# Kernel optimization log

Measured on AMD Instinct MI355X. Metric: run time of the kernel, lower is better.

Reference implementation:

```python
import jax, jax.numpy as jnp
import numpy as np

N, E, G, L = 50000, 800000, 256, 3
D, NF, EF, OUT = 300, 128, 16, 128
BN_EPS = 1e-5


def setup_inputs() -> dict:
    key = jax.random.key(0)
    ks = jax.random.split(key, 24)
    s = 0.02
    inp = {
        "node_feat": jax.random.normal(ks[0], (N, NF), jnp.float32),
        "edge_feat": jax.random.normal(ks[1], (E, EF), jnp.float32),
        "src": jax.random.randint(ks[2], (E,), 0, N),
        "dst": jax.random.randint(ks[3], (E,), 0, N),
        "graph_ids": jnp.sort(jax.random.randint(ks[4], (N,), 0, G)),
        "num_graphs": G,
        # encoder params
        "node_W": jax.random.normal(ks[5], (NF, D), jnp.float32) * s,
        "node_b": jnp.zeros((D,), jnp.float32),
        # per-layer edge encoders [L, EF, D]
        "edge_W": jax.random.normal(ks[6], (L, EF, D), jnp.float32) * s,
        "edge_b": jnp.zeros((L, D), jnp.float32),
        # per-layer GINEConv MLP: Linear(D,2D) BN ReLU Linear(2D,D) BN
        "W1": jax.random.normal(ks[7], (L, D, 2 * D), jnp.float32) * s,
        "b1": jnp.zeros((L, 2 * D), jnp.float32),
        "g1": jnp.ones((L, 2 * D), jnp.float32),
        "beta1": jnp.zeros((L, 2 * D), jnp.float32),
        "W2": jax.random.normal(ks[8], (L, 2 * D, D), jnp.float32) * s,
        "b2": jnp.zeros((L, D), jnp.float32),
        "g2": jnp.ones((L, D), jnp.float32),
        "beta2": jnp.zeros((L, D), jnp.float32),
        # prediction head
        "pred_W": jax.random.normal(ks[9], (D, OUT), jnp.float32) * s,
        "pred_b": jnp.zeros((OUT,), jnp.float32),
    }
    return inp


def _bn(x, g, b):
    # BatchNorm1d in training mode: biased batch statistics
    m = jnp.mean(x, axis=0)
    v = jnp.var(x, axis=0)
    return (x - m) * jax.lax.rsqrt(v + BN_EPS) * g + b


def reference(node_feat, edge_feat, src, dst, graph_ids, num_graphs,
              node_W, node_b, edge_W, edge_b,
              W1, b1, g1, beta1, W2, b2, g2, beta2,
              pred_W, pred_b):
    n_nodes = node_feat.shape[0]
    n_layers = edge_W.shape[0]
    hn = node_feat @ node_W + node_b  # [N, D]
    for l in range(n_layers):
        he = edge_feat @ edge_W[l] + edge_b[l]            # [E, D]
        msg = jax.nn.relu(hn[src] + he)                   # gather + edge fuse
        agg = jax.ops.segment_sum(msg, dst, num_segments=n_nodes)
        h = hn + agg                                      # (1+eps)*h + agg, eps=0
        h = jax.nn.relu(_bn(h @ W1[l] + b1[l], g1[l], beta1[l]))
        h = _bn(h @ W2[l] + b2[l], g2[l], beta2[l])
        hn = jax.nn.relu(h) if l != n_layers - 1 else h   # dropout p=0 -> identity
    # AvgPooling over nodes per graph
    cnt = jax.ops.segment_sum(jnp.ones((n_nodes, 1), hn.dtype), graph_ids,
                              num_segments=num_graphs)
    hg = jax.ops.segment_sum(hn, graph_ids, num_segments=num_graphs)
    hg = hg / jnp.maximum(cnt, 1.0)
    return hg @ pred_W + pred_b  # [G, OUT]
```

## Files before the change

### kernel.cpp

```cpp
#include <hip/hip_runtime.h>
#include <hip/hip_fp16.h>

#define N_NODES 50000
#define N_EDGES 800000
#define N_GRAPHS 256
#define N_LAYERS 3
#define DIM 300
#define NFEAT 128
#define EFEAT 16
#define OUTD 128
#define BN_EPS 1e-5f
#define HSTRIDE 320

typedef __attribute__((ext_vector_type(8))) _Float16 hfrag8;
typedef __attribute__((ext_vector_type(4))) float facc4;
typedef __attribute__((ext_vector_type(4))) unsigned short us4;
typedef __attribute__((ext_vector_type(8))) unsigned short us8;
typedef __attribute__((ext_vector_type(4))) unsigned int ui4;

__device__ __forceinline__ unsigned short f2bf(float f) {
    unsigned u = __float_as_uint(f);
    unsigned r = ((u >> 16) & 1u) + 0x7fffu;
    return (unsigned short)((u + r) >> 16);
}
__device__ __forceinline__ float bf2f(unsigned short h) {
    return __uint_as_float(((unsigned)h) << 16);
}
__device__ __forceinline__ unsigned short f2h(float f) {
    return __half_as_ushort(__float2half(f));
}
__device__ __forceinline__ float h2f(unsigned short u) {
    return __half2float(__ushort_as_half(u));
}

#if __has_builtin(__builtin_amdgcn_fdot2_f32_bf16)
#define GATHER_DOT2 1
typedef __attribute__((ext_vector_type(2))) __bf16 bf16x2_t;
__device__ __forceinline__ float dot2bf(unsigned a, unsigned b, float c) {
    return __builtin_amdgcn_fdot2_f32_bf16(
        __builtin_bit_cast(bf16x2_t, a), __builtin_bit_cast(bf16x2_t, b), c, false);
}
#else
#define GATHER_DOT2 0
#endif

__device__ __forceinline__ void load_lds16(const void* gsrc, void* ldsdst) {
    __builtin_amdgcn_global_load_lds(
        (const __attribute__((address_space(1))) unsigned int*)gsrc,
        (__attribute__((address_space(3))) unsigned int*)ldsdst,
        16, 0, 0);
}

#define MFMAH(a, b, c) __builtin_amdgcn_mfma_f32_16x16x32_f16(a, b, c, 0, 0, 0)

__global__ __launch_bounds__(256) void toh4(
    const float* __restrict__ x, unsigned short* __restrict__ H, int n4)
{
    int i = blockIdx.x * 256 + threadIdx.x;
    if (i >= n4) return;
    float4 v = ((const float4*)x)[i];
    us4 h;
    h.x = f2h(v.x); h.y = f2h(v.y); h.z = f2h(v.z); h.w = f2h(v.w);
    ((us4*)H)[i] = h;
}

__global__ __launch_bounds__(256) void toh_row(
    const float* __restrict__ hn, unsigned short* __restrict__ hnb)
{
    int i = blockIdx.x * 256 + threadIdx.x;
    if (i >= N_NODES * 80) return;
    int row = i / 80;
    int q = i - row * 80;
    us4 o;
    if (q < 75) {
        float4 v = *(const float4*)&hn[(size_t)row * DIM + 4 * q];
        o.x = f2h(v.x); o.y = f2h(v.y); o.z = f2h(v.z); o.w = f2h(v.w);
    } else {
        o.x = 0; o.y = 0; o.z = 0; o.w = 0;
    }
    *(us4*)&hnb[(size_t)row * HSTRIDE + 4 * q] = o;
}

__global__ __launch_bounds__(256) void conv_wt(
    const float* __restrict__ W, unsigned short* __restrict__ H,
    int K, int N, int Kp, int Np)
{
    int idx = blockIdx.x * 256 + threadIdx.x;
    if (idx >= Np * Kp) return;
    int n = idx / Kp;
    int k = idx - n * Kp;
    float v = (n < N && k < K) ? W[(size_t)k * N + n] : 0.f;
    H[idx] = f2h(v);
}

__global__ __launch_bounds__(256, 2) void gemm_pp(
    const unsigned short* __restrict__ Ah, const unsigned short* __restrict__ Bt,
    const float* __restrict__ bias, float* __restrict__ C,
    int M, int N, int Kp, float* __restrict__ stats)
{
    __shared__ unsigned short lds[8192];
    const int tid = threadIdx.x;
    const int lane = tid & 63;
    const int w = tid >> 6;
    const int m0 = blockIdx.y * 128;
    const int n0 = blockIdx.x * 128;
    const int wm = (w & 1) * 64;
    const int wn = (w >> 1) * 64;

    const int srow = lane >> 2;
    const int scol = (lane & 3) * 8;

    const unsigned short* gp[4];
    unsigned loff[4];
#pragma unroll
    for (int i = 0; i < 4; ++i) {
        int c = w * 4 + i;
        const unsigned short* pl = (c < 8) ? Ah : Bt;
        int rowg;
        if (c < 8) {
            rowg = m0 + (c & 7) * 16 + srow;
            rowg = min(rowg, M - 1);
        } else {
            rowg = n0 + (c & 7) * 16 + srow;
        }
        gp[i] = pl + (size_t)rowg * Kp + scol;
        loff[i] = c * 512;
    }

    facc4 acc[4][4];
    facc4 zero = {0.f, 0.f, 0.f, 0.f};
#pragma unroll
    for (int i = 0; i < 4; ++i)
#pragma unroll
        for (int j = 0; j < 4; ++j) acc[i][j] = zero;

    const int fr = lane & 15;
    const int fq = (lane >> 4) * 8;

    for (int k0 = 0; k0 < Kp; k0 += 32) {
#pragma unroll
        for (int i = 0; i < 4; ++i) {
            load_lds16(gp[i], &lds[loff[i]]);
            gp[i] += 32;
        }
        __syncthreads();

        hfrag8 ah[4], bh[4];
#pragma unroll
        for (int t = 0; t < 4; ++t) {
            int ar = wm + t * 16 + fr;
            ah[t] = *(const hfrag8*)&lds[ar * 32 + fq];
            int br = wn + t * 16 + fr;
            bh[t] = *(const hfrag8*)&lds[4096 + br * 32 + fq];
        }
#pragma unroll
        for (int i = 0; i < 4; ++i)
#pragma unroll
            for (int j = 0; j < 4; ++j)
                acc[i][j] = MFMAH(ah[i], bh[j], acc[i][j]);
        __syncthreads();
    }

#pragma unroll
    for (int i = 0; i < 4; ++i)
#pragma unroll
        for (int j = 0; j < 4; ++j) {
            int col = n0 + wn + j * 16 + (lane & 15);
            if (col >= N) continue;
            float bv = bias[col];
#pragma unroll
            for (int r = 0; r < 4; ++r) {
                int row = m0 + wm + i * 16 + (lane >> 4) * 4 + r;
                if (row < M)
                    C[(size_t)row * N + col] = acc[i][j][r] + bv;
            }
        }

    if (stats != nullptr) {
#pragma unroll
        for (int j = 0; j < 4; ++j) {
            int col = n0 + wn + j * 16 + (lane & 15);
            float cs = 0.f, cq = 0.f;
            if (col < N) {
                float bv = bias[col];
#pragma unroll
                for (int i = 0; i < 4; ++i)
#pragma unroll
                    for (int r = 0; r < 4; ++r) {
                        int row = m0 + wm + i * 16 + (lane >> 4) * 4 + r;
                        if (row < M) {
                            float y = acc[i][j][r] + bv;
                            cs += y;
                            cq = fmaf(y, y, cq);
                        }
                    }
            }
            cs += __shfl_xor(cs, 16, 64); cq += __shfl_xor(cq, 16, 64);
            cs += __shfl_xor(cs, 32, 64); cq += __shfl_xor(cq, 32, 64);
            if ((lane >> 4) == 0 && col < N) {
                atomicAdd(&stats[col], cs);
                atomicAdd(&stats[N + col], cq);
            }
        }
    }
}

__global__ __launch_bounds__(256, 2) void gemm_af(
    const float* __restrict__ A, const unsigned short* __restrict__ Bt,
    const float* __restrict__ bias, float* __restrict__ C,
    int M, int N, int K, int Kp,
    const float* __restrict__ abn, float* __restrict__ stats)
{
    __shared__ unsigned short lds[8192];
    const int tid = threadIdx.x;
    const int lane = tid & 63;
    const int w = tid >> 6;
    const int m0 = blockIdx.y * 128;
    const int n0 = blockIdx.x * 128;
    const int wm = (w & 1) * 64;
    const int wn = (w >> 1) * 64;

    const int srow = lane >> 2;
    const int scol = (lane & 3) * 8;

    const unsigned short* gpb[2];
    unsigned loffb[2];
#pragma unroll
    for (int i = 0; i < 2; ++i) {
        int c = w * 2 + i;
        int rowg = n0 + c * 16 + srow;
        gpb[i] = Bt + (size_t)rowg * Kp + scol;
        loffb[i] = 4096 + c * 512;
    }

    facc4 acc[4][4];
    facc4 zero = {0.f, 0.f, 0.f, 0.f};
#pragma unroll
    for (int i = 0; i < 4; ++i)
#pragma unroll
        for (int j = 0; j < 4; ++j) acc[i][j] = zero;

    const int fr = lane & 15;
    const int fq = (lane >> 4) * 8;

    for (int k0 = 0; k0 < Kp; k0 += 32) {
#pragma unroll
        for (int i = 0; i < 2; ++i) {
            load_lds16(gpb[i], &lds[loffb[i]]);
            gpb[i] += 32;
        }
#pragma unroll
        for (int i = 0; i < 4; ++i) {
            int idx = tid + i * 256;
            int row = idx >> 3;
            int q4 = idx & 7;
            int rg = min(m0 + row, M - 1);
            int kk = k0 + q4 * 4;
            us4 h;
            if (kk < K) {
                float4 v = *(const float4*)&A[(size_t)rg * K + kk];
                float4 sa = *(const float4*)&abn[kk];
                float4 sb = *(const float4*)&abn[K + kk];
                h.x = f2h(fmaxf(fmaf(v.x, sa.x, sb.x), 0.f));
                h.y = f2h(fmaxf(fmaf(v.y, sa.y, sb.y), 0.f));
                h.z = f2h(fmaxf(fmaf(v.z, sa.z, sb.z), 0.f));
                h.w = f2h(fmaxf(fmaf(v.w, sa.w, sb.w), 0.f));
            } else {
                h.x = 0; h.y = 0; h.z = 0; h.w = 0;
            }
            *(us4*)&lds[row * 32 + q4 * 4] = h;
        }
        __syncthreads();

        hfrag8 ah[4], bh[4];
#pragma unroll
        for (int t = 0; t < 4; ++t) {
            int ar = wm + t * 16 + fr;
            ah[t] = *(const hfrag8*)&lds[ar * 32 + fq];
            int br = wn + t * 16 + fr;
            bh[t] = *(const hfrag8*)&lds[4096 + br * 32 + fq];
        }
#pragma unroll
        for (int i = 0; i < 4; ++i)
#pragma unroll
            for (int j = 0; j < 4; ++j)
                acc[i][j] = MFMAH(ah[i], bh[j], acc[i][j]);
        __syncthreads();
    }

#pragma unroll
    for (int i = 0; i < 4; ++i)
#pragma unroll
        for (int j = 0; j < 4; ++j) {
            int col = n0 + wn + j * 16 + (lane & 15);
            if (col >= N) continue;
            float bv = bias[col];
#pragma unroll
            for (int r = 0; r < 4; ++r) {
                int row = m0 + wm + i * 16 + (lane >> 4) * 4 + r;
                if (row < M)
                    C[(size_t)row * N + col] = acc[i][j][r] + bv;
            }
        }

    if (stats != nullptr) {
#pragma unroll
        for (int j = 0; j < 4; ++j) {
            int col = n0 + wn + j * 16 + (lane & 15);
            float cs = 0.f, cq = 0.f;
            if (col < N) {
                float bv = bias[col];
#pragma unroll
                for (int i = 0; i < 4; ++i)
#pragma unroll
                    for (int r = 0; r < 4; ++r) {
                        int row = m0 + wm + i * 16 + (lane >> 4) * 4 + r;
                        if (row < M) {
                            float y = acc[i][j][r] + bv;
                            cs += y;
                            cq = fmaf(y, y, cq);
                        }
                    }
            }
            cs += __shfl_xor(cs, 16, 64); cq += __shfl_xor(cq, 16, 64);
            cs += __shfl_xor(cs, 32, 64); cq += __shfl_xor(cq, 32, 64);
            if ((lane >> 4) == 0 && col < N) {
                atomicAdd(&stats[col], cs);
                atomicAdd(&stats[N + col], cq);
            }
        }
    }
}

__global__ __launch_bounds__(256) void csr_count(const int* __restrict__ dst, int* __restrict__ P)
{
    int e = blockIdx.x * 256 + threadIdx.x;
    if (e < N_EDGES) atomicAdd(&P[dst[e] + 1], 1);
}

__global__ __launch_bounds__(1024) void csr_scan(int* __restrict__ P)
{
    __shared__ int part[1024];
    const int t = threadIdx.x;
    const int CH = 49;
    int i0 = t * CH;
    int s = 0;
    for (int i = i0; i < i0 + CH; ++i) {
        if (i <= N_NODES) { s += P[i]; P[i] = s; }
    }
    part[t] = s;
    __syncthreads();
    if (t == 0) {
        int run = 0;
        for (int k = 0; k < 1024; ++k) { int tmp = part[k]; part[k] = run; run += tmp; }
    }
    __syncthreads();
    int off = part[t];
    for (int i = i0; i < i0 + CH; ++i) {
        if (i <= N_NODES) P[i] += off;
    }
}

__global__ __launch_bounds__(256) void csr_fill(
    const int* __restrict__ dst, int* __restrict__ P, int* __restrict__ eids)
{
    int e = blockIdx.x * 256 + threadIdx.x;
    if (e < N_EDGES) {
        int pos = atomicAdd(&P[dst[e]], 1);
        eids[pos] = e;
    }
}

__global__ __launch_bounds__(256) void edge_pack_bf(
    const int* __restrict__ src, const int* __restrict__ eids,
    const float* __restrict__ edge_feat, int* __restrict__ es,
    unsigned short* __restrict__ efsb)
{
    int j = blockIdx.x * 256 + threadIdx.x;
    if (j >= N_EDGES) return;
    int e = eids[j];
    es[j] = src[e];
    const float* sp = edge_feat + (size_t)e * EFEAT;
    us8 o0, o1;
#pragma unroll
    for (int k = 0; k < 8; ++k) {
        o0[k] = f2bf(sp[k]);
        o1[k] = f2bf(sp[8 + k]);
    }
    *(us8*)&efsb[(size_t)j * EFEAT] = o0;
    *(us8*)&efsb[(size_t)j * EFEAT + 8] = o1;
}

__global__ __launch_bounds__(256) void gather_agg7(
    const unsigned short* __restrict__ hnb, const unsigned short* __restrict__ efsb,
    const int* __restrict__ es, const int* __restrict__ P,
    const float* __restrict__ eW, const float* __restrict__ eb,
    unsigned short* __restrict__ aggH)
{
    const int v = blockIdx.x * 4 + (threadIdx.x >> 6);
    if (v >= N_NODES) return;
    const int lane = threadIdx.x & 63;

    float acc[5];
    float ebv[5];
    {
        us4 r4 = *(const us4*)&hnb[(size_t)v * HSTRIDE + 4 * lane];
        acc[0] = h2f(r4.x); acc[1] = h2f(r4.y);
        acc[2] = h2f(r4.z); acc[3] = h2f(r4.w);
        acc[4] = h2f(hnb[(size_t)v * HSTRIDE + 256 + lane]);
    }
#if GATHER_DOT2
    unsigned wpk[8][5];
#pragma unroll
    for (int q = 0; q < 5; ++q) {
        int d = (q < 4) ? 4 * lane + q : 256 + lane;
        bool dv = d < DIM;
        ebv[q] = dv ? eb[d] : 0.f;
#pragma unroll
        for (int p = 0; p < 8; ++p) {
            unsigned short h0 = dv ? f2bf(eW[(2 * p) * DIM + d]) : (unsigned short)0;
            unsigned short h1 = dv ? f2bf(eW[(2 * p + 1) * DIM + d]) : (unsigned short)0;
            wpk[p][q] = (unsigned)h0 | ((unsigned)h1 << 16);
        }
    }
#else
    float wr[EFEAT][5];
#pragma unroll
    for (int q = 0; q < 5; ++q) {
        int d = (q < 4) ? 4 * lane + q : 256 + lane;
        bool dv = d < DIM;
        ebv[q] = dv ? eb[d] : 0.f;
#pragma unroll
        for (int k = 0; k < EFEAT; ++k)
            wr[k][q] = dv ? eW[k * DIM + d] : 0.f;
    }
#endif

    const int j0 = (v == 0) ? 0 : P[v - 1];
    const int j1 = P[v];

    int j = j0;
    for (; j + 4 <= j1; j += 4) {
        int s0 = __builtin_amdgcn_readfirstlane(es[j]);
        int s1 = __builtin_amdgcn_readfirstlane(es[j + 1]);
        int s2 = __builtin_amdgcn_readfirstlane(es[j + 2]);
        int s3 = __builtin_amdgcn_readfirstlane(es[j + 3]);
        const unsigned short* __restrict__ h0 = hnb + (size_t)s0 * HSTRIDE;
        const unsigned short* __restrict__ h1 = hnb + (size_t)s1 * HSTRIDE;
        const unsigned short* __restrict__ h2p = hnb + (size_t)s2 * HSTRIDE;
        const unsigned short* __restrict__ h3 = hnb + (size_t)s3 * HSTRIDE;
        us4 r4[4];
        unsigned short r1[4];
        r4[0] = *(const us4*)&h0[4 * lane];  r1[0] = h0[256 + lane];
        r4[1] = *(const us4*)&h1[4 * lane];  r1[1] = h1[256 + lane];
        r4[2] = *(const us4*)&h2p[4 * lane]; r1[2] = h2p[256 + lane];
        r4[3] = *(const us4*)&h3[4 * lane];  r1[3] = h3[256 + lane];
#if GATHER_DOT2
        ui4 pa[4][2];
#pragma unroll
        for (int u = 0; u < 4; ++u) {
            pa[u][0] = *(const ui4*)&efsb[(size_t)(j + u) * EFEAT];
            pa[u][1] = *(const ui4*)&efsb[(size_t)(j + u) * EFEAT + 8];
        }
#pragma unroll
        for (int u = 0; u < 4; ++u) {
            float hv[5];
            hv[0] = h2f(r4[u][0]); hv[1] = h2f(r4[u][1]);
            hv[2] = h2f(r4[u][2]); hv[3] = h2f(r4[u][3]);
            hv[4] = h2f(r1[u]);
#pragma unroll
            for (int q = 0; q < 5; ++q) {
                float he = ebv[q];
                he = dot2bf(pa[u][0][0], wpk[0][q], he);
                he = dot2bf(pa[u][0][1], wpk[1][q], he);
                he = dot2bf(pa[u][0][2], wpk[2][q], he);
                he = dot2bf(pa[u][0][3], wpk[3][q], he);
                he = dot2bf(pa[u][1][0], wpk[4][q], he);
                he = dot2bf(pa[u][1][1], wpk[5][q], he);
                he = dot2bf(pa[u][1][2], wpk[6][q], he);
                he = dot2bf(pa[u][1][3], wpk[7][q], he);
                acc[q] += fmaxf(hv[q] + he, 0.f);
            }
        }
#else
        us8 pk[4][2];
#pragma unroll
        for (int u = 0; u < 4; ++u) {
            pk[u][0] = *(const us8*)&efsb[(size_t)(j + u) * EFEAT];
            pk[u][1] = *(const us8*)&efsb[(size_t)(j + u) * EFEAT + 8];
        }
#pragma unroll
        for (int u = 0; u < 4; ++u) {
            float hv[5];
            hv[0] = h2f(r4[u][0]); hv[1] = h2f(r4[u][1]);
            hv[2] = h2f(r4[u][2]); hv[3] = h2f(r4[u][3]);
            hv[4] = h2f(r1[u]);
            float ef[EFEAT];
#pragma unroll
            for (int k = 0; k < 8; ++k) {
                ef[k] = bf2f(pk[u][0][k]);
                ef[8 + k] = bf2f(pk[u][1][k]);
            }
#pragma unroll
            for (int q = 0; q < 5; ++q) {
                float he = ebv[q];
#pragma unroll
                for (int k = 0; k < EFEAT; ++k) he = fmaf(ef[k], wr[k][q], he);
                acc[q] += fmaxf(hv[q] + he, 0.f);
            }
        }
#endif
    }
    for (; j < j1; ++j) {
        int s = __builtin_amdgcn_readfirstlane(es[j]);
        const unsigned short* __restrict__ hp = hnb + (size_t)s * HSTRIDE;
        us4 r4 = *(const us4*)&hp[4 * lane];
        unsigned short r1 = hp[256 + lane];
        float hv[5];
        hv[0] = h2f(r4.x); hv[1] = h2f(r4.y);
        hv[2] = h2f(r4.z); hv[3] = h2f(r4.w);
        hv[4] = h2f(r1);
#if GATHER_DOT2
        ui4 p0 = *(const ui4*)&efsb[(size_t)j * EFEAT];
        ui4 p1 = *(const ui4*)&efsb[(size_t)j * EFEAT + 8];
#pragma unroll
        for (int q = 0; q < 5; ++q) {
            float he = ebv[q];
            he = dot2bf(p0[0], wpk[0][q], he);
            he = dot2bf(p0[1], wpk[1][q], he);
            he = dot2bf(p0[2], wpk[2][q], he);
            he = dot2bf(p0[3], wpk[3][q], he);
            he = dot2bf(p1[0], wpk[4][q], he);
            he = dot2bf(p1[1], wpk[5][q], he);
            he = dot2bf(p1[2], wpk[6][q], he);
            he = dot2bf(p1[3], wpk[7][q], he);
            acc[q] += fmaxf(hv[q] + he, 0.f);
        }
#else
        us8 p0 = *(const us8*)&efsb[(size_t)j * EFEAT];
        us8 p1 = *(const us8*)&efsb[(size_t)j * EFEAT + 8];
        float ef[EFEAT];
#pragma unroll
        for (int k = 0; k < 8; ++k) {
            ef[k] = bf2f(p0[k]);
            ef[8 + k] = bf2f(p1[k]);
        }
#pragma unroll
        for (int q = 0; q < 5; ++q) {
            float he = ebv[q];
#pragma unroll
            for (int k = 0; k < EFEAT; ++k) he = fmaf(ef[k], wr[k][q], he);
            acc[q] += fmaxf(hv[q] + he, 0.f);
        }
#endif
    }

    {
        us4 o;
        o.x = f2h(acc[0]); o.y = f2h(acc[1]);
        o.z = f2h(acc[2]); o.w = f2h(acc[3]);
        *(us4*)&aggH[(size_t)v * 320 + 4 * lane] = o;
        aggH[(size_t)v * 320 + 256 + lane] = f2h(acc[4]);
    }
}

__global__ __launch_bounds__(256) void bn_finalize(
    const float* __restrict__ stats, const float* __restrict__ g,
    const float* __restrict__ beta, float* __restrict__ ab, int C)
{
    int c = blockIdx.x * 256 + threadIdx.x;
    if (c >= C) return;
    const float invN = 1.f / (float)N_NODES;
    float m = stats[c] * invN;
    float v = stats[C + c] * invN - m * m;
    float a = g[c] * rsqrtf(v + BN_EPS);
    ab[c] = a;
    ab[C + c] = beta[c] - m * a;
}

__global__ __launch_bounds__(256) void bn_apply_h(
    const float* __restrict__ x, const float* __restrict__ ab,
    unsigned short* __restrict__ hnb)
{
    int i = blockIdx.x * 256 + threadIdx.x;
    if (i >= N_NODES * 80) return;
    int row = i / 80;
    int q = i - row * 80;
    int c = 4 * q;
    us4 o;
    if (q < 75) {
        float4 v = ((const float4*)x)[row * 75 + q];
        const float* a = ab + c;
        const float* bb = ab + DIM + c;
        o.x = f2h(fmaxf(fmaf(v.x, a[0], bb[0]), 0.f));
        o.y = f2h(fmaxf(fmaf(v.y, a[1], bb[1]), 0.f));
        o.z = f2h(fmaxf(fmaf(v.z, a[2], bb[2]), 0.f));
        o.w = f2h(fmaxf(fmaf(v.w, a[3], bb[3]), 0.f));
    } else {
        o.x = 0; o.y = 0; o.z = 0; o.w = 0;
    }
    *(us4*)&hnb[(size_t)row * HSTRIDE + c] = o;
}

__global__ __launch_bounds__(256) void pool_seg_bn(
    const float* __restrict__ h2, const int* __restrict__ gid,
    const float* __restrict__ ab, float* __restrict__ hg)
{
    const int g = blockIdx.x;
    int lo = 0, hi = N_NODES;
    while (lo < hi) { int mid = (lo + hi) >> 1; if (gid[mid] < g) lo = mid + 1; else hi = mid; }
    int lo2 = lo, hi2 = N_NODES;
    while (lo2 < hi2) { int mid = (lo2 + hi2) >> 1; if (gid[mid] < g + 1) lo2 = mid + 1; else hi2 = mid; }
    const float inv = 1.f / fmaxf((float)(lo2 - lo), 1.f);
    for (int d = threadIdx.x; d < DIM; d += 256) {
        float s = 0.f;
        for (int r = lo; r < lo2; ++r) s += h2[(size_t)r * DIM + d];
        hg[(size_t)g * DIM + d] = fmaf(s * inv, ab[d], ab[DIM + d]);
    }
}

#define TS 64
#define BK 16
#define ASP 68

__global__ __launch_bounds__(256) void sgemm_bias(
    const float* __restrict__ A, const float* __restrict__ B,
    const float* __restrict__ bias, float* __restrict__ C,
    int M, int Ncol, int K)
{
    __shared__ float As[BK][ASP];
    __shared__ float Bs[BK][TS];
    const int tid = threadIdx.x;
    const int bm = blockIdx.x * TS;
    const int bn = blockIdx.y * TS;
    const int tm = (tid >> 4) * 4;
    const int tn = (tid & 15) * 4;
    float acc[4][4] = {};

    for (int k0 = 0; k0 < K; k0 += BK) {
#pragma unroll
        for (int i = 0; i < 4; ++i) {
            int idx = tid + i * 256;
            int m = idx >> 4;
            int k = idx & 15;
            int row = bm + m, kk = k0 + k;
            float v = 0.f;
            if (row < M && kk < K) v = A[(size_t)row * K + kk];
            As[k][m] = v;
        }
#pragma unroll
        for (int i = 0; i < 4; ++i) {
            int idx = tid + i * 256;
            int k = idx >> 6;
            int n = idx & 63;
            int col = bn + n, kk = k0 + k;
            float v = 0.f;
            if (col < Ncol && kk < K) v = B[(size_t)kk * Ncol + col];
            Bs[k][n] = v;
        }
        __syncthreads();
#pragma unroll
        for (int k = 0; k < BK; ++k) {
            float4 av = *(const float4*)&As[k][tm];
            float4 bv = *(const float4*)&Bs[k][tn];
            float a4[4] = {av.x, av.y, av.z, av.w};
            float b4[4] = {bv.x, bv.y, bv.z, bv.w};
#pragma unroll
            for (int i = 0; i < 4; ++i)
#pragma unroll
                for (int j = 0; j < 4; ++j)
                    acc[i][j] = fmaf(a4[i], b4[j], acc[i][j]);
        }
        __syncthreads();
    }

#pragma unroll
    for (int i = 0; i < 4; ++i) {
        int row = bm + tm + i;
        if (row >= M) continue;
#pragma unroll
        for (int j = 0; j < 4; ++j) {
            int col = bn + tn + j;
            if (col < Ncol)
                C[(size_t)row * Ncol + col] = acc[i][j] + bias[col];
        }
    }
}

extern "C" void kernel_launch(void* const* d_in, const int* in_sizes, int n_in,
                              void* d_out, int out_size, void* d_ws, size_t ws_size,
                              hipStream_t stream)
{
    const float* node_feat = (const float*)d_in[0];
    const float* edge_feat = (const float*)d_in[1];
    const int*   src       = (const int*)d_in[2];
    const int*   dst       = (const int*)d_in[3];
    const int*   gid       = (const int*)d_in[4];
    const float* node_W = (const float*)d_in[6];
    const float* node_b = (const float*)d_in[7];
    const float* edge_W = (const float*)d_in[8];
    const float* edge_b = (const float*)d_in[9];
    const float* W1  = (const float*)d_in[10];
    const float* b1  = (const float*)d_in[11];
    const float* g1  = (const float*)d_in[12];
    const float* be1 = (const float*)d_in[13];
    const float* W2  = (const float*)d_in[14];
    const float* b2  = (const float*)d_in[15];
    const float* g2  = (const float*)d_in[16];
    const float* be2 = (const float*)d_in[17];
    const float* pred_W = (const float*)d_in[18];
    const float* pred_b = (const float*)d_in[19];
    float* out = (float*)d_out;

    char* base = (char*)d_ws;
    float* hn            = (float*)(base + 0);
    float* h2            = hn;
    float* x1            = (float*)(base + 60000000);
    unsigned short* nfH  = (unsigned short*)x1;
    unsigned short* hnb  = (unsigned short*)x1;
    unsigned short* aggH = (unsigned short*)(base + 180000000);
    int*   es            = (int*)(base + 212000000);
    unsigned short* efsb = (unsigned short*)(base + 215200000);
    unsigned short* wtH  = (unsigned short*)(base + 244000000);
    int*   eids          = (int*)(base + 245000000);
    int*   P             = (int*)(base + 248200000);
    float* stats         = (float*)(base + 248400016);
    float* ab            = (float*)(base + 248407216);
    float* hg            = (float*)(base + 248414416);
    float* stats2        = stats + 1200;
    float* ab2           = ab + 1200;

    dim3 blk(256);

    toh4<<<dim3((N_NODES * NFEAT / 4 + 255) / 256), blk, 0, stream>>>(
        node_feat, nfH, N_NODES * NFEAT / 4);
    conv_wt<<<dim3((384 * 128 + 255) / 256), blk, 0, stream>>>(
        node_W, wtH, NFEAT, DIM, 128, 384);
    gemm_pp<<<dim3(3, 391), blk, 0, stream>>>(
        nfH, wtH, node_b, hn, N_NODES, DIM, 128, nullptr);
    toh_row<<<dim3((N_NODES * 80 + 255) / 256), blk, 0, stream>>>(hn, hnb);

    hipMemsetAsync(P, 0, (N_NODES + 1) * sizeof(int), stream);
    csr_count<<<dim3((N_EDGES + 255) / 256), blk, 0, stream>>>(dst, P);
    csr_scan<<<dim3(1), dim3(1024), 0, stream>>>(P);
    csr_fill<<<dim3((N_EDGES + 255) / 256), blk, 0, stream>>>(dst, P, eids);
    edge_pack_bf<<<dim3((N_EDGES + 255) / 256), blk, 0, stream>>>(
        src, eids, edge_feat, es, efsb);

    for (int l = 0; l < N_LAYERS; ++l) {
        gather_agg7<<<dim3((N_NODES + 3) / 4), blk, 0, stream>>>(
            hnb, efsb, es, P,
            edge_W + (size_t)l * EFEAT * DIM, edge_b + (size_t)l * DIM, aggH);

        hipMemsetAsync(stats, 0, 1800 * sizeof(float), stream);

        conv_wt<<<dim3((640 * 320 + 255) / 256), blk, 0, stream>>>(
            W1 + (size_t)l * DIM * 2 * DIM, wtH, DIM, 2 * DIM, 320, 640);
        gemm_pp<<<dim3(5, 391), blk, 0, stream>>>(
            aggH, wtH, b1 + (size_t)l * 2 * DIM, x1,
            N_NODES, 2 * DIM, 320, stats);
        bn_finalize<<<dim3(3), blk, 0, stream>>>(
            stats, g1 + (size_t)l * 2 * DIM, be1 + (size_t)l * 2 * DIM, ab, 2 * DIM);

        conv_wt<<<dim3((384 * 608 + 255) / 256), blk, 0, stream>>>(
            W2 + (size_t)l * 2 * DIM * DIM, wtH, 2 * DIM, DIM, 608, 384);
        gemm_af<<<dim3(3, 391), blk, 0, stream>>>(
            x1, wtH, b2 + (size_t)l * DIM, h2, N_NODES, DIM, 2 * DIM, 608,
            ab, stats2);
        bn_finalize<<<dim3(2), blk, 0, stream>>>(
            stats2, g2 + (size_t)l * DIM, be2 + (size_t)l * DIM, ab2, DIM);

        if (l < N_LAYERS - 1)
            bn_apply_h<<<dim3((N_NODES * 80 + 255) / 256), blk, 0, stream>>>(
                h2, ab2, hnb);
    }

    pool_seg_bn<<<dim3(N_GRAPHS), blk, 0, stream>>>(h2, gid, ab2, hg);
    sgemm_bias<<<dim3((N_GRAPHS + 63) / 64, (OUTD + 63) / 64), blk, 0, stream>>>(
        hg, pred_W, pred_b, out, N_GRAPHS, OUTD, DIM);
}
```

Baseline: 1.850 ms.

## Store GEMM intermediates in fp16 and fuse input encoder output conversion

The GEMM kernels now write their outputs (x1, h2, encoder output) as fp16 instead of fp32. The consumers (gemm_af, bn_apply_h, pool_seg_bn) read these fp16 buffers and convert to float on load. The encoder GEMM writes straight into the padded fp16 hnb buffer, so the separate toh_row conversion kernel is removed. This roughly halves the memory traffic for the large intermediates, at the cost of rounding the pre-BN activations to fp16. The batch-norm statistics are still computed from the fp32 accumulators.

```diff
diff --git a/kernel.cpp b/kernel.cpp
--- a/kernel.cpp
+++ b/kernel.cpp
@@ -64,23 +64,6 @@
     ((us4*)H)[i] = h;
 }
 
-__global__ __launch_bounds__(256) void toh_row(
-    const float* __restrict__ hn, unsigned short* __restrict__ hnb)
-{
-    int i = blockIdx.x * 256 + threadIdx.x;
-    if (i >= N_NODES * 80) return;
-    int row = i / 80;
-    int q = i - row * 80;
-    us4 o;
-    if (q < 75) {
-        float4 v = *(const float4*)&hn[(size_t)row * DIM + 4 * q];
-        o.x = f2h(v.x); o.y = f2h(v.y); o.z = f2h(v.z); o.w = f2h(v.w);
-    } else {
-        o.x = 0; o.y = 0; o.z = 0; o.w = 0;
-    }
-    *(us4*)&hnb[(size_t)row * HSTRIDE + 4 * q] = o;
-}
-
 __global__ __launch_bounds__(256) void conv_wt(
     const float* __restrict__ W, unsigned short* __restrict__ H,
     int K, int N, int Kp, int Np)
@@ -95,8 +78,8 @@
 
 __global__ __launch_bounds__(256, 2) void gemm_pp(
     const unsigned short* __restrict__ Ah, const unsigned short* __restrict__ Bt,
-    const float* __restrict__ bias, float* __restrict__ C,
-    int M, int N, int Kp, float* __restrict__ stats)
+    const float* __restrict__ bias, unsigned short* __restrict__ Ch,
+    int M, int N, int Kp, int ldh, float* __restrict__ stats)
 {
     __shared__ unsigned short lds[8192];
     const int tid = threadIdx.x;
@@ -166,13 +149,13 @@
 #pragma unroll
         for (int j = 0; j < 4; ++j) {
             int col = n0 + wn + j * 16 + (lane & 15);
-            if (col >= N) continue;
-            float bv = bias[col];
+            if (col >= ldh) continue;
+            float bv = (col < N) ? bias[col] : 0.f;
 #pragma unroll
             for (int r = 0; r < 4; ++r) {
                 int row = m0 + wm + i * 16 + (lane >> 4) * 4 + r;
                 if (row < M)
-                    C[(size_t)row * N + col] = acc[i][j][r] + bv;
+                    Ch[(size_t)row * ldh + col] = f2h(acc[i][j][r] + bv);
             }
         }
 
@@ -206,8 +189,8 @@
 }
 
 __global__ __launch_bounds__(256, 2) void gemm_af(
-    const float* __restrict__ A, const unsigned short* __restrict__ Bt,
-    const float* __restrict__ bias, float* __restrict__ C,
+    const unsigned short* __restrict__ A, const unsigned short* __restrict__ Bt,
+    const float* __restrict__ bias, unsigned short* __restrict__ Ch,
     int M, int N, int K, int Kp,
     const float* __restrict__ abn, float* __restrict__ stats)
 {
@@ -258,13 +241,13 @@
             int kk = k0 + q4 * 4;
             us4 h;
             if (kk < K) {
-                float4 v = *(const float4*)&A[(size_t)rg * K + kk];
+                us4 v = *(const us4*)&A[(size_t)rg * K + kk];
                 float4 sa = *(const float4*)&abn[kk];
                 float4 sb = *(const float4*)&abn[K + kk];
-                h.x = f2h(fmaxf(fmaf(v.x, sa.x, sb.x), 0.f));
-                h.y = f2h(fmaxf(fmaf(v.y, sa.y, sb.y), 0.f));
-                h.z = f2h(fmaxf(fmaf(v.z, sa.z, sb.z), 0.f));
-                h.w = f2h(fmaxf(fmaf(v.w, sa.w, sb.w), 0.f));
+                h.x = f2h(fmaxf(fmaf(h2f(v.x), sa.x, sb.x), 0.f));
+                h.y = f2h(fmaxf(fmaf(h2f(v.y), sa.y, sb.y), 0.f));
+                h.z = f2h(fmaxf(fmaf(h2f(v.z), sa.z, sb.z), 0.f));
+                h.w = f2h(fmaxf(fmaf(h2f(v.w), sa.w, sb.w), 0.f));
             } else {
                 h.x = 0; h.y = 0; h.z = 0; h.w = 0;
             }
@@ -299,7 +282,7 @@
             for (int r = 0; r < 4; ++r) {
                 int row = m0 + wm + i * 16 + (lane >> 4) * 4 + r;
                 if (row < M)
-                    C[(size_t)row * N + col] = acc[i][j][r] + bv;
+                    Ch[(size_t)row * N + col] = f2h(acc[i][j][r] + bv);
             }
         }
 
@@ -579,7 +562,7 @@
 }
 
 __global__ __launch_bounds__(256) void bn_apply_h(
-    const float* __restrict__ x, const float* __restrict__ ab,
+    const unsigned short* __restrict__ x, const float* __restrict__ ab,
     unsigned short* __restrict__ hnb)
 {
     int i = blockIdx.x * 256 + threadIdx.x;
@@ -589,13 +572,13 @@
     int c = 4 * q;
     us4 o;
     if (q < 75) {
-        float4 v = ((const float4*)x)[row * 75 + q];
+        us4 v = *(const us4*)&x[(size_t)row * DIM + c];
         const float* a = ab + c;
         const float* bb = ab + DIM + c;
-        o.x = f2h(fmaxf(fmaf(v.x, a[0], bb[0]), 0.f));
-        o.y = f2h(fmaxf(fmaf(v.y, a[1], bb[1]), 0.f));
-        o.z = f2h(fmaxf(fmaf(v.z, a[2], bb[2]), 0.f));
-        o.w = f2h(fmaxf(fmaf(v.w, a[3], bb[3]), 0.f));
+        o.x = f2h(fmaxf(fmaf(h2f(v.x), a[0], bb[0]), 0.f));
+        o.y = f2h(fmaxf(fmaf(h2f(v.y), a[1], bb[1]), 0.f));
+        o.z = f2h(fmaxf(fmaf(h2f(v.z), a[2], bb[2]), 0.f));
+        o.w = f2h(fmaxf(fmaf(h2f(v.w), a[3], bb[3]), 0.f));
     } else {
         o.x = 0; o.y = 0; o.z = 0; o.w = 0;
     }
@@ -603,7 +586,7 @@
 }
 
 __global__ __launch_bounds__(256) void pool_seg_bn(
-    const float* __restrict__ h2, const int* __restrict__ gid,
+    const unsigned short* __restrict__ h2, const int* __restrict__ gid,
     const float* __restrict__ ab, float* __restrict__ hg)
 {
     const int g = blockIdx.x;
@@ -614,7 +597,7 @@
     const float inv = 1.f / fmaxf((float)(lo2 - lo), 1.f);
     for (int d = threadIdx.x; d < DIM; d += 256) {
         float s = 0.f;
-        for (int r = lo; r < lo2; ++r) s += h2[(size_t)r * DIM + d];
+        for (int r = lo; r < lo2; ++r) s += h2f(h2[(size_t)r * DIM + d]);
         hg[(size_t)g * DIM + d] = fmaf(s * inv, ab[d], ab[DIM + d]);
     }
 }
@@ -713,12 +696,11 @@
     float* out = (float*)d_out;
 
     char* base = (char*)d_ws;
-    float* hn            = (float*)(base + 0);
-    float* h2            = hn;
-    float* x1            = (float*)(base + 60000000);
-    unsigned short* nfH  = (unsigned short*)x1;
-    unsigned short* hnb  = (unsigned short*)x1;
+    unsigned short* h2h  = (unsigned short*)(base + 0);
+    unsigned short* x1h  = (unsigned short*)(base + 60000000);
+    unsigned short* hnb  = x1h;
     unsigned short* aggH = (unsigned short*)(base + 180000000);
+    unsigned short* nfH  = aggH;
     int*   es            = (int*)(base + 212000000);
     unsigned short* efsb = (unsigned short*)(base + 215200000);
     unsigned short* wtH  = (unsigned short*)(base + 244000000);
@@ -737,8 +719,7 @@
     conv_wt<<<dim3((384 * 128 + 255) / 256), blk, 0, stream>>>(
         node_W, wtH, NFEAT, DIM, 128, 384);
     gemm_pp<<<dim3(3, 391), blk, 0, stream>>>(
-        nfH, wtH, node_b, hn, N_NODES, DIM, 128, nullptr);
-    toh_row<<<dim3((N_NODES * 80 + 255) / 256), blk, 0, stream>>>(hn, hnb);
+        nfH, wtH, node_b, hnb, N_NODES, DIM, 128, HSTRIDE, nullptr);
 
     hipMemsetAsync(P, 0, (N_NODES + 1) * sizeof(int), stream);
     csr_count<<<dim3((N_EDGES + 255) / 256), blk, 0, stream>>>(dst, P);
@@ -757,25 +738,25 @@
         conv_wt<<<dim3((640 * 320 + 255) / 256), blk, 0, stream>>>(
             W1 + (size_t)l * DIM * 2 * DIM, wtH, DIM, 2 * DIM, 320, 640);
         gemm_pp<<<dim3(5, 391), blk, 0, stream>>>(
-            aggH, wtH, b1 + (size_t)l * 2 * DIM, x1,
-            N_NODES, 2 * DIM, 320, stats);
+            aggH, wtH, b1 + (size_t)l * 2 * DIM, x1h,
+            N_NODES, 2 * DIM, 320, 600, stats);
         bn_finalize<<<dim3(3), blk, 0, stream>>>(
             stats, g1 + (size_t)l * 2 * DIM, be1 + (size_t)l * 2 * DIM, ab, 2 * DIM);
 
         conv_wt<<<dim3((384 * 608 + 255) / 256), blk, 0, stream>>>(
             W2 + (size_t)l * 2 * DIM * DIM, wtH, 2 * DIM, DIM, 608, 384);
         gemm_af<<<dim3(3, 391), blk, 0, stream>>>(
-            x1, wtH, b2 + (size_t)l * DIM, h2, N_NODES, DIM, 2 * DIM, 608,
+            x1h, wtH, b2 + (size_t)l * DIM, h2h, N_NODES, DIM, 2 * DIM, 608,
             ab, stats2);
         bn_finalize<<<dim3(2), blk, 0, stream>>>(
             stats2, g2 + (size_t)l * DIM, be2 + (size_t)l * DIM, ab2, DIM);
 
         if (l < N_LAYERS - 1)
             bn_apply_h<<<dim3((N_NODES * 80 + 255) / 256), blk, 0, stream>>>(
-                h2, ab2, hnb);
-    }
-
-    pool_seg_bn<<<dim3(N_GRAPHS), blk, 0, stream>>>(h2, gid, ab2, hg);
+                h2h, ab2, hnb);
+    }
+
+    pool_seg_bn<<<dim3(N_GRAPHS), blk, 0, stream>>>(h2h, gid, ab2, hg);
     sgemm_bias<<<dim3((N_GRAPHS + 63) / 64, (OUTD + 63) / 64), blk, 0, stream>>>(
         hg, pred_W, pred_b, out, N_GRAPHS, OUTD, DIM);
 }
```

Result: faster. 1.766 ms (-4.5%).
